# Performance work log

Hardware: AMD Instinct MI355X
Metric: run time of the kernel (lower is better)

Reference implementation:

```python
import jax, jax.numpy as jnp
import numpy as np

STRIDES = (8, 16, 32)
BINS = 16
NC = 80
ALPHA, GAMMA = 0.25, 2.0
W_CLS, W_IOU, W_DFL = 1.0, 7.5, 1.5
B, MAX_GT = 32, 32
EPS = 1e-7


def setup_inputs() -> dict:
    key = jax.random.key(0)
    k0, k1, k2, k3, k4, k5, k6 = jax.random.split(key, 7)
    p0 = jax.random.normal(k0, (B, 4 * BINS + NC, 80, 80), dtype=jnp.float32)
    p1 = jax.random.normal(k1, (B, 4 * BINS + NC, 40, 40), dtype=jnp.float32)
    p2 = jax.random.normal(k2, (B, 4 * BINS + NC, 20, 20), dtype=jnp.float32)
    # realistic xyxy boxes inside a 640x640 image
    c = jax.random.uniform(k3, (B, MAX_GT, 2), minval=60.0, maxval=580.0)
    wh = jax.random.uniform(k4, (B, MAX_GT, 2), minval=16.0, maxval=120.0)
    gt_bboxes = jnp.concatenate([c - wh / 2, c + wh / 2], axis=-1).astype(jnp.float32)
    gt_labels = jax.random.randint(k5, (B, MAX_GT), 0, NC, dtype=jnp.int32)
    raw = jax.random.randint(k6, (B, 8400), 0, 20 * MAX_GT, dtype=jnp.int32)
    matched_gt_inds = jnp.where(raw < MAX_GT, raw, -1)
    return {"p0": p0, "p1": p1, "p2": p2, "gt_bboxes": gt_bboxes,
            "gt_labels": gt_labels, "matched_gt_inds": matched_gt_inds}


def _decode_scale(p, stride):
    # p: [B, 4*BINS + NC, H, W]
    Bp, C, H, W = p.shape
    dfl = p[:, :4 * BINS].reshape(Bp, 4, BINS, H, W)
    cls = p[:, 4 * BINS:]
    # DFL decode: expectation of softmax over bins, scaled by stride
    prob = jax.nn.softmax(dfl, axis=2)
    proj = jnp.arange(BINS, dtype=p.dtype)
    dist = jnp.einsum('bkchw,c->bkhw', prob, proj) * stride  # [B,4,H,W] in pixels
    ys, xs = jnp.meshgrid(jnp.arange(H), jnp.arange(W), indexing='ij')
    cx = ((xs.astype(p.dtype)) + 0.5) * stride
    cy = ((ys.astype(p.dtype)) + 0.5) * stride
    boxes = jnp.stack([cx - dist[:, 0], cy - dist[:, 1],
                       cx + dist[:, 2], cy + dist[:, 3]], axis=-1).reshape(Bp, H * W, 4)
    cls_logits = cls.transpose(0, 2, 3, 1).reshape(Bp, H * W, NC)
    dfl_flat = dfl.transpose(0, 3, 4, 1, 2).reshape(Bp, H * W, 4, BINS)
    grid = jnp.stack([cx, cy], axis=-1).reshape(H * W, 2)
    smap = jnp.full((H * W,), stride, dtype=p.dtype)
    return cls_logits, dfl_flat, boxes, grid, smap


def reference(p0, p1, p2, gt_bboxes, gt_labels, matched_gt_inds):
    outs = [_decode_scale(p, s) for p, s in zip((p0, p1, p2), STRIDES)]
    scores = jnp.concatenate([o[0] for o in outs], axis=1)   # [B,N,NC]
    dfl = jnp.concatenate([o[1] for o in outs], axis=1)      # [B,N,4,BINS]
    pboxes = jnp.concatenate([o[2] for o in outs], axis=1)   # [B,N,4]
    grid = jnp.concatenate([o[3] for o in outs], axis=0)     # [N,2]
    smap = jnp.concatenate([o[4] for o in outs], axis=0)     # [N]

    pos = matched_gt_inds >= 0                               # [B,N]
    idx = jnp.where(pos, matched_gt_inds, 0)
    lbl = jnp.take_along_axis(gt_labels, idx, axis=1)        # [B,N]
    posf = pos.astype(scores.dtype)
    tgt_scores = jax.nn.one_hot(lbl, NC, dtype=scores.dtype) * posf[..., None]

    # sigmoid focal loss (stable BCE-with-logits)
    prob = jax.nn.sigmoid(scores)
    ce = jnp.maximum(scores, 0) - scores * tgt_scores + jnp.log1p(jnp.exp(-jnp.abs(scores)))
    p_t = prob * tgt_scores + (1 - prob) * (1 - tgt_scores)
    alpha_t = tgt_scores * ALPHA + (1 - tgt_scores) * (1 - ALPHA)
    cls_elem = alpha_t * (1.0 - p_t) ** GAMMA * ce
    num_pos = jnp.maximum(posf.sum(), 1.0)
    loss_cls = cls_elem.sum() / num_pos

    # gather matched GT boxes per anchor
    tboxes = jnp.take_along_axis(gt_bboxes, idx[..., None], axis=1)  # [B,N,4]
    gx, gy = grid[None, :, 0], grid[None, :, 1]
    l = jnp.clip(gx - tboxes[..., 0], 0.0)
    t = jnp.clip(gy - tboxes[..., 1], 0.0)
    r = jnp.clip(tboxes[..., 2] - gx, 0.0)
    b_ = jnp.clip(tboxes[..., 3] - gy, 0.0)
    dists = jnp.stack([l, t, r, b_], axis=-1) / smap[None, :, None]   # [B,N,4]
    tb = jnp.clip(dists, 0.0, BINS - 1 - 1e-6)
    lo = jnp.floor(tb).astype(jnp.int32)
    hi = jnp.minimum(lo + 1, BINS - 1)
    a = tb - lo.astype(tb.dtype)
    # soft two-bin DFL target (vectorized form of the scatter_add loop)
    tdist = (jax.nn.one_hot(lo, BINS, dtype=dfl.dtype) * (1.0 - a)[..., None]
             + jax.nn.one_hot(hi, BINS, dtype=dfl.dtype) * a[..., None])   # [B,N,4,BINS]
    logp = jax.nn.log_softmax(dfl, axis=-1)
    dfl_elem = -(tdist * logp).sum(-1)                                # [B,N,4]
    loss_dfl = (dfl_elem * posf[..., None]).sum() / (num_pos * 4.0)

    # IoU loss on positives
    ix1 = jnp.maximum(pboxes[..., 0], tboxes[..., 0])
    iy1 = jnp.maximum(pboxes[..., 1], tboxes[..., 1])
    ix2 = jnp.minimum(pboxes[..., 2], tboxes[..., 2])
    iy2 = jnp.minimum(pboxes[..., 3], tboxes[..., 3])
    inter = jnp.clip(ix2 - ix1, 0.0) * jnp.clip(iy2 - iy1, 0.0)
    area_p = jnp.clip(pboxes[..., 2] - pboxes[..., 0], 0.0) * jnp.clip(pboxes[..., 3] - pboxes[..., 1], 0.0)
    area_t = jnp.clip(tboxes[..., 2] - tboxes[..., 0], 0.0) * jnp.clip(tboxes[..., 3] - tboxes[..., 1], 0.0)
    iou = inter / (area_p + area_t - inter + EPS)
    loss_iou = ((1.0 - iou) * posf).sum() / num_pos

    total = W_CLS * loss_cls + W_IOU * loss_iou + W_DFL * loss_dfl
    return total
```

## Files before the change

### kernel.cpp

```cpp
#include <hip/hip_runtime.h>
#include <math.h>

#define NCLS 80
#define BINS 16
#define BATCH 32
#define MAX_GT 32
#define NA 8400
#define AN (BATCH * NA)
#define NT 2100
#define GRID 2048
#define NU_DFL 2100
#define NU_CLS 5280
#define NVB (NU_DFL + NU_CLS)
#define NROWS (GRID * 2)
#define NSLOT 64
#define ALPHA_C 0.25f
#define W_CLS 1.0
#define W_IOU 7.5
#define W_DFL 1.5
#define EPS_F 1e-7f

__device__ __forceinline__ float focal0(float s)
{
    float e  = __expf(-s);
    float t  = 1.f + e;
    float r  = __builtin_amdgcn_rcpf(t);
    float lg = __logf(t);
    return 0.75f * r * r * (s + lg);
}

__device__ __forceinline__ float focal_corr(float s)
{
    float e  = __expf(-s);
    float t  = 1.f + e;
    float r  = __builtin_amdgcn_rcpf(t);
    float lg = __logf(t);
    return r * r * (0.25f * e * e * lg - 0.75f * (s + lg));
}

__device__ __forceinline__ void wave_write4(float c0, float c1, float c2, float c3,
                                            double* __restrict__ blk)
{
    #pragma unroll
    for (int o = 32; o > 0; o >>= 1) {
        c0 += __shfl_down(c0, o);
        c1 += __shfl_down(c1, o);
        c2 += __shfl_down(c2, o);
        c3 += __shfl_down(c3, o);
    }
    const int lane = (int)threadIdx.x & 63;
    if (lane == 0) {
        const int row = (int)blockIdx.x * 2 + ((int)threadIdx.x >> 6);
        double* o = blk + (size_t)row * 4;
        o[0] = (double)c0; o[1] = (double)c1; o[2] = (double)c2; o[3] = (double)c3;
    }
}

template<int HW, int SSTR, int WQ>
__device__ __forceinline__ void dfl_scale(
    const float* __restrict__ p, int b, int tl, int k, int gbase, int tid,
    const float* __restrict__ gt_bboxes, const int* __restrict__ gt_labels,
    const int* __restrict__ matched,
    float& c_cls, float& c_iou, float& c_dfl, float& c_cnt)
{
    const float stride = (float)SSTR;
    const float inv_s  = 1.f / stride;
    const int h  = tl / WQ;
    const int w0 = (tl - h * WQ) * 4;
    const int off = tl * 4;
    const float cy = ((float)h + 0.5f) * stride;
    const float* pc = p + (size_t)(b * 144 + k * BINS) * HW + off;

    float4 v[BINS];
    #pragma unroll
    for (int i = 0; i < BINS; ++i)
        v[i] = *(const float4*)(pc + (size_t)(i * HW));
    const int4 m4 = *(const int4*)(matched + (size_t)b * NA + gbase + off);
    const int mm[4] = {m4.x, m4.y, m4.z, m4.w};

    float se[4] = {0.f, 0.f, 0.f, 0.f}, we[4] = {0.f, 0.f, 0.f, 0.f};
    #pragma unroll
    for (int i = 0; i < BINS; ++i) {
        const float wgt = (float)i;
        float e0 = __expf(v[i].x), e1 = __expf(v[i].y);
        float e2 = __expf(v[i].z), e3 = __expf(v[i].w);
        se[0] += e0; we[0] = fmaf(wgt, e0, we[0]);
        se[1] += e1; we[1] = fmaf(wgt, e1, we[1]);
        se[2] += e2; we[2] = fmaf(wgt, e2, we[2]);
        se[3] += e3; we[3] = fmaf(wgt, e3, we[3]);
    }

    float pd[4];
    #pragma unroll
    for (int j = 0; j < 4; ++j) pd[j] = (we[j] / se[j]) * stride;

    #pragma unroll
    for (int j = 0; j < 4; ++j) {
        if (mm[j] >= 0) {
            const float4 tb = *(const float4*)(gt_bboxes + ((size_t)b * MAX_GT + mm[j]) * 4);
            const float cx = ((float)(w0 + j) + 0.5f) * stride;
            float d = (k == 0) ? (cx - tb.x) : (k == 1) ? (cy - tb.y)
                    : (k == 2) ? (tb.z - cx) : (tb.w - cy);
            float tval = fminf(fmaxf(d, 0.f) * inv_s, (float)(BINS - 1) - 1e-6f);
            int   lo = (int)tval;
            float fr = tval - (float)lo;
            float vlo = pc[(size_t)(lo * HW) + j];
            float vhi = pc[(size_t)((lo + 1) * HW) + j];
            float lse = __logf(se[j]);
            c_dfl += -((1.f - fr) * (vlo - lse) + fr * (vhi - lse));
        }
    }

    const int lbase = (tid & 63) & ~3;
    float d1[4], d2[4], d3[4];
    #pragma unroll
    for (int j = 0; j < 4; ++j) {
        d1[j] = __shfl(pd[j], lbase + 1);
        d2[j] = __shfl(pd[j], lbase + 2);
        d3[j] = __shfl(pd[j], lbase + 3);
    }
    if (k == 0) {
        #pragma unroll
        for (int j = 0; j < 4; ++j) {
            if (mm[j] >= 0) {
                const float cx = ((float)(w0 + j) + 0.5f) * stride;
                float px1 = cx - pd[j], py1 = cy - d1[j];
                float px2 = cx + d2[j], py2 = cy + d3[j];
                const float4 tb = *(const float4*)(gt_bboxes + ((size_t)b * MAX_GT + mm[j]) * 4);
                float ix1 = fmaxf(px1, tb.x), iy1 = fmaxf(py1, tb.y);
                float ix2 = fminf(px2, tb.z), iy2 = fminf(py2, tb.w);
                float inter  = fmaxf(ix2 - ix1, 0.f) * fmaxf(iy2 - iy1, 0.f);
                float area_p = fmaxf(px2 - px1, 0.f) * fmaxf(py2 - py1, 0.f);
                float area_t = fmaxf(tb.z - tb.x, 0.f) * fmaxf(tb.w - tb.y, 0.f);
                float iou = inter / (area_p + area_t - inter + EPS_F);
                c_iou += 1.f - iou;
                c_cnt += 1.f;
                int lbl = gt_labels[b * MAX_GT + mm[j]];
                float sv = *(p + (size_t)(b * 144 + 4 * BINS + lbl) * HW + off + j);
                c_cls += focal_corr(sv);
            }
        }
    }
}

__global__ __launch_bounds__(128, 4) void yolo_mega(
    const float* __restrict__ p0, const float* __restrict__ p1, const float* __restrict__ p2,
    const float* __restrict__ gt_bboxes, const int* __restrict__ gt_labels,
    const int* __restrict__ matched, double* __restrict__ blk)
{
    const int tid = (int)threadIdx.x;
    float c_cls = 0.f, c_iou = 0.f, c_dfl = 0.f, c_cnt = 0.f;

    for (int vb = (int)blockIdx.x; vb < NVB; vb += GRID) {
        if (vb < NU_DFL) {
            const int gdt = vb * 128 + tid;
            const int k   = gdt & 3;
            const int qg  = gdt >> 2;
            const int b   = qg / NT;
            const int t   = qg - b * NT;
            if (t < 1600)
                dfl_scale<6400,  8, 20>(p0, b, t,        k, 0,    tid,
                                        gt_bboxes, gt_labels, matched, c_cls, c_iou, c_dfl, c_cnt);
            else if (t < 2000)
                dfl_scale<1600, 16, 10>(p1, b, t - 1600, k, 6400, tid,
                                        gt_bboxes, gt_labels, matched, c_cls, c_iou, c_dfl, c_cnt);
            else
                dfl_scale< 400, 32,  5>(p2, b, t - 2000, k, 8000, tid,
                                        gt_bboxes, gt_labels, matched, c_cls, c_iou, c_dfl, c_cnt);
        } else {
            const int c = vb - NU_DFL;
            const int b = c / 165;
            const int r = c - b * 165;
            const float* base; int len, off;
            if (r < 125)      { base = p0 + (size_t)b * 921600 + 409600; len = 512000; off = r * 4096; }
            else if (r < 157) { base = p1 + (size_t)b * 230400 + 102400; len = 128000; off = (r - 125) * 4096; }
            else              { base = p2 + (size_t)b * 57600  + 25600;  len = 32000;  off = (r - 157) * 4096; }

            float4 q[8]; bool val[8];
            #pragma unroll
            for (int i = 0; i < 8; ++i) {
                int o = off + i * 512 + tid * 4;
                val[i] = (o < len);
                q[i] = *(const float4*)(base + (val[i] ? o : 0));
            }
            float part = 0.f;
            #pragma unroll
            for (int i = 0; i < 8; ++i) {
                float s = focal0(q[i].x) + focal0(q[i].y) + focal0(q[i].z) + focal0(q[i].w);
                part += val[i] ? s : 0.f;
            }
            c_cls += part;
        }
    }
    wave_write4(c_cls, c_iou, c_dfl, c_cnt, blk);
}

__global__ __launch_bounds__(1024) void yolo_finalize_blocks(
    const double* __restrict__ blk, float* __restrict__ out)
{
    const int tid = (int)threadIdx.x;
    double s0 = 0.0, s1 = 0.0, s2 = 0.0, s3 = 0.0;
    #pragma unroll
    for (int r = tid; r < NROWS; r += 1024) {
        const double2* rp = (const double2*)(blk + (size_t)r * 4);
        double2 a = rp[0], b = rp[1];
        s0 += a.x; s1 += a.y; s2 += b.x; s3 += b.y;
    }
    #pragma unroll
    for (int o = 32; o > 0; o >>= 1) {
        s0 += __shfl_down(s0, o); s1 += __shfl_down(s1, o);
        s2 += __shfl_down(s2, o); s3 += __shfl_down(s3, o);
    }
    __shared__ double sh[16][4];
    const int wave = tid >> 6, lane = tid & 63;
    if (lane == 0) { sh[wave][0] = s0; sh[wave][1] = s1; sh[wave][2] = s2; sh[wave][3] = s3; }
    __syncthreads();
    if (tid == 0) {
        double c = 0, i = 0, d = 0, n = 0;
        for (int w = 0; w < 16; ++w) { c += sh[w][0]; i += sh[w][1]; d += sh[w][2]; n += sh[w][3]; }
        double np = (n < 1.0) ? 1.0 : n;
        out[0] = (float)(W_CLS * c / np + W_IOU * i / np + W_DFL * d / (np * 4.0));
    }
}

__device__ __forceinline__ void block_reduce_atomic(float val, double* __restrict__ target)
{
    __shared__ float s[4];
    __syncthreads();
    #pragma unroll
    for (int o = 32; o > 0; o >>= 1) val += __shfl_down(val, o);
    const int wave = threadIdx.x >> 6, lane = threadIdx.x & 63;
    if (lane == 0) s[wave] = val;
    __syncthreads();
    if (threadIdx.x == 0) atomicAdd(target, (double)(s[0] + s[1] + s[2] + s[3]));
}

__device__ __forceinline__ float focal_elem(float s, float tt)
{
    float e   = __expf(-fabsf(s));
    float inv = 1.f / (1.f + e);
    float prob = (s >= 0.f) ? inv : e * inv;
    float ce  = fmaxf(s, 0.f) - s * tt + __logf(1.f + e);
    float p_t = prob * tt + (1.f - prob) * (1.f - tt);
    float alpha_t = tt * ALPHA_C + (1.f - tt) * (1.f - ALPHA_C);
    float om = 1.f - p_t;
    return alpha_t * om * om * ce;
}

__global__ __launch_bounds__(256) void yolo_loss_fused(
    const float* __restrict__ p0, const float* __restrict__ p1, const float* __restrict__ p2,
    const float* __restrict__ gt_bboxes, const int* __restrict__ gt_labels,
    const int* __restrict__ matched, double* __restrict__ acc)
{
    const int a = blockIdx.x * blockDim.x + threadIdx.x;
    const int b = blockIdx.y;
    const int slot = blockIdx.x & (NSLOT - 1);
    float cls_acc = 0.f, iou_acc = 0.f, dfl_acc = 0.f, pos_cnt = 0.f;
    if (a < NA) {
        const float* p; int HW, W; float stride; int off;
        if (a < 6400)      { p = p0; HW = 6400; W = 80; stride = 8.f;  off = a; }
        else if (a < 8000) { p = p1; HW = 1600; W = 40; stride = 16.f; off = a - 6400; }
        else               { p = p2; HW = 400;  W = 20; stride = 32.f; off = a - 8000; }
        const int h = off / W, w = off - h * W;
        const float cx = ((float)w + 0.5f) * stride, cy = ((float)h + 0.5f) * stride;
        const float* pb = p + ((size_t)b * 144) * (size_t)HW + (size_t)off;
        const int m = matched[(size_t)b * NA + a];
        const bool pos = (m >= 0);
        const int idx = pos ? m : 0;
        const int lbl = gt_labels[b * MAX_GT + idx];
        const float* tbp = gt_bboxes + ((size_t)b * MAX_GT + idx) * 4;
        const float tx1 = tbp[0], ty1 = tbp[1], tx2 = tbp[2], ty2 = tbp[3];
        float tdist[4] = {fmaxf(cx - tx1, 0.f) / stride, fmaxf(cy - ty1, 0.f) / stride,
                          fmaxf(tx2 - cx, 0.f) / stride, fmaxf(ty2 - cy, 0.f) / stride};
        float pdv[4]; float dfl_sum = 0.f;
        #pragma unroll
        for (int k = 0; k < 4; ++k) {
            float tv = fminf(tdist[k], (float)(BINS - 1) - 1e-6f);
            int lo = (int)floorf(tv);
            float fr = tv - (float)lo;
            const float* pcx = pb + (size_t)(k * BINS) * HW;
            float v[BINS];
            #pragma unroll
            for (int i = 0; i < BINS; ++i) v[i] = pcx[(size_t)i * HW];
            float mx = v[0];
            #pragma unroll
            for (int i = 1; i < BINS; ++i) mx = fmaxf(mx, v[i]);
            float se = 0.f, we = 0.f, vlo = 0.f, vhi = 0.f;
            #pragma unroll
            for (int i = 0; i < BINS; ++i) {
                float e = __expf(v[i] - mx);
                se += e; we += (float)i * e;
                vlo = (i == lo) ? v[i] : vlo;
                vhi = (i == lo + 1) ? v[i] : vhi;
            }
            pdv[k] = (we / se) * stride;
            if (pos) { float lse = mx + __logf(se); dfl_sum += -((1.f - fr) * (vlo - lse) + fr * (vhi - lse)); }
        }
        const float* pcls = pb + (size_t)(4 * BINS) * HW;
        #pragma unroll 4
        for (int c = 0; c < NCLS; ++c)
            cls_acc += focal_elem(pcls[(size_t)c * HW], (pos && c == lbl) ? 1.f : 0.f);
        if (pos) {
            float px1 = cx - pdv[0], py1 = cy - pdv[1], px2 = cx + pdv[2], py2 = cy + pdv[3];
            float ix1 = fmaxf(px1, tx1), iy1 = fmaxf(py1, ty1);
            float ix2 = fminf(px2, tx2), iy2 = fminf(py2, ty2);
            float inter  = fmaxf(ix2 - ix1, 0.f) * fmaxf(iy2 - iy1, 0.f);
            float area_p = fmaxf(px2 - px1, 0.f) * fmaxf(py2 - py1, 0.f);
            float area_t = fmaxf(tx2 - tx1, 0.f) * fmaxf(ty2 - ty1, 0.f);
            float iou = inter / (area_p + area_t - inter + EPS_F);
            iou_acc = 1.f - iou; dfl_acc = dfl_sum; pos_cnt = 1.f;
        }
    }
    block_reduce_atomic(cls_acc, &acc[0 * NSLOT + slot]);
    block_reduce_atomic(iou_acc, &acc[1 * NSLOT + slot]);
    block_reduce_atomic(dfl_acc, &acc[2 * NSLOT + slot]);
    block_reduce_atomic(pos_cnt, &acc[3 * NSLOT + slot]);
}

__global__ void yolo_loss_finalize(const double* __restrict__ acc, float* __restrict__ out)
{
    double s[4] = {0.0, 0.0, 0.0, 0.0};
    for (int q = 0; q < 4; ++q)
        for (int i = 0; i < NSLOT; ++i) s[q] += acc[q * NSLOT + i];
    double np = s[3] < 1.0 ? 1.0 : s[3];
    double total = W_CLS * s[0] / np + W_IOU * s[1] / np + W_DFL * s[2] / (np * 4.0);
    out[0] = (float)total;
}

extern "C" void kernel_launch(void* const* d_in, const int* in_sizes, int n_in,
                              void* d_out, int out_size, void* d_ws, size_t ws_size,
                              hipStream_t stream)
{
    const float* p0        = (const float*)d_in[0];
    const float* p1        = (const float*)d_in[1];
    const float* p2        = (const float*)d_in[2];
    const float* gt_bboxes = (const float*)d_in[3];
    const int*   gt_labels = (const int*)d_in[4];
    const int*   matched   = (const int*)d_in[5];
    float*  out = (float*)d_out;

    const size_t need = (size_t)NROWS * 4 * sizeof(double);

    if (ws_size >= need) {
        double* blk = (double*)d_ws;
        yolo_mega<<<GRID, 128, 0, stream>>>(p0, p1, p2, gt_bboxes, gt_labels, matched, blk);
        yolo_finalize_blocks<<<1, 1024, 0, stream>>>(blk, out);
    } else {
        double* acc = (double*)d_ws;
        (void)hipMemsetAsync(acc, 0, 4 * NSLOT * sizeof(double), stream);
        dim3 g((NA + 255) / 256, BATCH);
        yolo_loss_fused<<<g, 256, 0, stream>>>(p0, p1, p2, gt_bboxes, gt_labels, matched, acc);
        yolo_loss_finalize<<<1, 1, 0, stream>>>(acc, out);
    }
}
```

Measured before the change: 219.0 us.

## Split cls and positive kernels, skip DFL loads for all-negative anchor quads

Separates the dense classification focal sum into its own kernel with a flat grid-stride float4 mapping. The positive-anchor kernel now reads matched indices first and returns early when all four anchors in a quad are negative, which avoids the 16-bin DFL loads for most anchors. Block reductions go through shared memory to one row per block. This adds an extra kernel launch, and the branch divergence in the positive kernel may leave some bandwidth unused.

```diff
diff --git a/kernel.cpp b/kernel.cpp
--- a/kernel.cpp
+++ b/kernel.cpp
@@ -6,13 +6,7 @@
 #define BATCH 32
 #define MAX_GT 32
 #define NA 8400
-#define AN (BATCH * NA)
 #define NT 2100
-#define GRID 2048
-#define NU_DFL 2100
-#define NU_CLS 5280
-#define NVB (NU_DFL + NU_CLS)
-#define NROWS (GRID * 2)
 #define NSLOT 64
 #define ALPHA_C 0.25f
 #define W_CLS 1.0
@@ -20,6 +14,14 @@
 #define W_DFL 1.5
 #define EPS_F 1e-7f
 
+#define IMG_Q4 168000u
+#define CLS_Q4 5376000u
+#define CLS_GRID 2048
+#define CLS_STRIDE (CLS_GRID * 256)
+
+#define POS_GRID 1050
+#define NROWS (CLS_GRID + POS_GRID)
+
 __device__ __forceinline__ float focal0(float s)
 {
     float e  = __expf(-s);
@@ -38,8 +40,8 @@
     return r * r * (0.25f * e * e * lg - 0.75f * (s + lg));
 }
 
-__device__ __forceinline__ void wave_write4(float c0, float c1, float c2, float c3,
-                                            double* __restrict__ blk)
+__device__ __forceinline__ void block_write4(float c0, float c1, float c2, float c3,
+                                             double* __restrict__ row)
 {
     #pragma unroll
     for (int o = 32; o > 0; o >>= 1) {
@@ -48,26 +50,74 @@
         c2 += __shfl_down(c2, o);
         c3 += __shfl_down(c3, o);
     }
-    const int lane = (int)threadIdx.x & 63;
-    if (lane == 0) {
-        const int row = (int)blockIdx.x * 2 + ((int)threadIdx.x >> 6);
-        double* o = blk + (size_t)row * 4;
-        o[0] = (double)c0; o[1] = (double)c1; o[2] = (double)c2; o[3] = (double)c3;
-    }
+    __shared__ float s4[4][4];
+    const int wave = threadIdx.x >> 6, lane = threadIdx.x & 63;
+    if (lane == 0) { s4[wave][0] = c0; s4[wave][1] = c1; s4[wave][2] = c2; s4[wave][3] = c3; }
+    __syncthreads();
+    if (threadIdx.x == 0) {
+        row[0] = (double)(s4[0][0] + s4[1][0] + s4[2][0] + s4[3][0]);
+        row[1] = (double)(s4[0][1] + s4[1][1] + s4[2][1] + s4[3][1]);
+        row[2] = (double)(s4[0][2] + s4[1][2] + s4[2][2] + s4[3][2]);
+        row[3] = (double)(s4[0][3] + s4[1][3] + s4[2][3] + s4[3][3]);
+    }
+}
+
+__device__ __forceinline__ const float4* cls_map(unsigned v,
+    const float4* q0, const float4* q1, const float4* q2)
+{
+    unsigned b  = v / IMG_Q4;
+    unsigned r  = v - b * IMG_Q4;
+    return (r < 128000u) ? (q0 + (size_t)b * 230400 + 102400 + r)
+         : (r < 160000u) ? (q1 + (size_t)b * 57600  + 25600  + (r - 128000u))
+                         : (q2 + (size_t)b * 14400  + 6400   + (r - 160000u));
+}
+
+__global__ __launch_bounds__(256) void yolo_cls(
+    const float* __restrict__ p0, const float* __restrict__ p1, const float* __restrict__ p2,
+    double* __restrict__ blk)
+{
+    const float4* q0 = (const float4*)p0;
+    const float4* q1 = (const float4*)p1;
+    const float4* q2 = (const float4*)p2;
+    const unsigned gtid = blockIdx.x * 256 + threadIdx.x;
+
+    float c = 0.f;
+    unsigned vi = gtid;
+    #pragma unroll
+    for (int rnd = 0; rnd < 2; ++rnd) {
+        float4 q[5];
+        #pragma unroll
+        for (int u = 0; u < 5; ++u)
+            q[u] = *cls_map(vi + u * CLS_STRIDE, q0, q1, q2);
+        #pragma unroll
+        for (int u = 0; u < 5; ++u)
+            c += (focal0(q[u].x) + focal0(q[u].y)) + (focal0(q[u].z) + focal0(q[u].w));
+        vi += 5 * CLS_STRIDE;
+    }
+    if (vi < CLS_Q4) {
+        float4 q = *cls_map(vi, q0, q1, q2);
+        c += (focal0(q.x) + focal0(q.y)) + (focal0(q.z) + focal0(q.w));
+    }
+    block_write4(c, 0.f, 0.f, 0.f, blk + (size_t)blockIdx.x * 4);
 }
 
 template<int HW, int SSTR, int WQ>
-__device__ __forceinline__ void dfl_scale(
+__device__ __forceinline__ void pos_scale(
     const float* __restrict__ p, int b, int tl, int k, int gbase, int tid,
     const float* __restrict__ gt_bboxes, const int* __restrict__ gt_labels,
     const int* __restrict__ matched,
     float& c_cls, float& c_iou, float& c_dfl, float& c_cnt)
 {
+    const int off = tl * 4;
+    const int4 m4 = *(const int4*)(matched + (size_t)b * NA + gbase + off);
+    const int mm[4] = {m4.x, m4.y, m4.z, m4.w};
+    const bool any = (mm[0] >= 0) | (mm[1] >= 0) | (mm[2] >= 0) | (mm[3] >= 0);
+    if (!any) return;
+
     const float stride = (float)SSTR;
     const float inv_s  = 1.f / stride;
     const int h  = tl / WQ;
     const int w0 = (tl - h * WQ) * 4;
-    const int off = tl * 4;
     const float cy = ((float)h + 0.5f) * stride;
     const float* pc = p + (size_t)(b * 144 + k * BINS) * HW + off;
 
@@ -75,8 +125,6 @@
     #pragma unroll
     for (int i = 0; i < BINS; ++i)
         v[i] = *(const float4*)(pc + (size_t)(i * HW));
-    const int4 m4 = *(const int4*)(matched + (size_t)b * NA + gbase + off);
-    const int mm[4] = {m4.x, m4.y, m4.z, m4.w};
 
     float se[4] = {0.f, 0.f, 0.f, 0.f}, we[4] = {0.f, 0.f, 0.f, 0.f};
     #pragma unroll
@@ -143,56 +191,30 @@
     }
 }
 
-__global__ __launch_bounds__(128, 4) void yolo_mega(
+__global__ __launch_bounds__(256) void yolo_pos(
     const float* __restrict__ p0, const float* __restrict__ p1, const float* __restrict__ p2,
     const float* __restrict__ gt_bboxes, const int* __restrict__ gt_labels,
     const int* __restrict__ matched, double* __restrict__ blk)
 {
     const int tid = (int)threadIdx.x;
+    const int gdt = (int)blockIdx.x * 256 + tid;
+    const int k   = gdt & 3;
+    const int qg  = gdt >> 2;
+    const int b   = qg / NT;
+    const int t   = qg - b * NT;
+
     float c_cls = 0.f, c_iou = 0.f, c_dfl = 0.f, c_cnt = 0.f;
-
-    for (int vb = (int)blockIdx.x; vb < NVB; vb += GRID) {
-        if (vb < NU_DFL) {
-            const int gdt = vb * 128 + tid;
-            const int k   = gdt & 3;
-            const int qg  = gdt >> 2;
-            const int b   = qg / NT;
-            const int t   = qg - b * NT;
-            if (t < 1600)
-                dfl_scale<6400,  8, 20>(p0, b, t,        k, 0,    tid,
-                                        gt_bboxes, gt_labels, matched, c_cls, c_iou, c_dfl, c_cnt);
-            else if (t < 2000)
-                dfl_scale<1600, 16, 10>(p1, b, t - 1600, k, 6400, tid,
-                                        gt_bboxes, gt_labels, matched, c_cls, c_iou, c_dfl, c_cnt);
-            else
-                dfl_scale< 400, 32,  5>(p2, b, t - 2000, k, 8000, tid,
-                                        gt_bboxes, gt_labels, matched, c_cls, c_iou, c_dfl, c_cnt);
-        } else {
-            const int c = vb - NU_DFL;
-            const int b = c / 165;
-            const int r = c - b * 165;
-            const float* base; int len, off;
-            if (r < 125)      { base = p0 + (size_t)b * 921600 + 409600; len = 512000; off = r * 4096; }
-            else if (r < 157) { base = p1 + (size_t)b * 230400 + 102400; len = 128000; off = (r - 125) * 4096; }
-            else              { base = p2 + (size_t)b * 57600  + 25600;  len = 32000;  off = (r - 157) * 4096; }
-
-            float4 q[8]; bool val[8];
-            #pragma unroll
-            for (int i = 0; i < 8; ++i) {
-                int o = off + i * 512 + tid * 4;
-                val[i] = (o < len);
-                q[i] = *(const float4*)(base + (val[i] ? o : 0));
-            }
-            float part = 0.f;
-            #pragma unroll
-            for (int i = 0; i < 8; ++i) {
-                float s = focal0(q[i].x) + focal0(q[i].y) + focal0(q[i].z) + focal0(q[i].w);
-                part += val[i] ? s : 0.f;
-            }
-            c_cls += part;
-        }
-    }
-    wave_write4(c_cls, c_iou, c_dfl, c_cnt, blk);
+    if (t < 1600)
+        pos_scale<6400,  8, 20>(p0, b, t,        k, 0,    tid,
+                                gt_bboxes, gt_labels, matched, c_cls, c_iou, c_dfl, c_cnt);
+    else if (t < 2000)
+        pos_scale<1600, 16, 10>(p1, b, t - 1600, k, 6400, tid,
+                                gt_bboxes, gt_labels, matched, c_cls, c_iou, c_dfl, c_cnt);
+    else
+        pos_scale< 400, 32,  5>(p2, b, t - 2000, k, 8000, tid,
+                                gt_bboxes, gt_labels, matched, c_cls, c_iou, c_dfl, c_cnt);
+
+    block_write4(c_cls, c_iou, c_dfl, c_cnt, blk + (size_t)(CLS_GRID + blockIdx.x) * 4);
 }
 
 __global__ __launch_bounds__(1024) void yolo_finalize_blocks(
@@ -200,7 +222,6 @@
 {
     const int tid = (int)threadIdx.x;
     double s0 = 0.0, s1 = 0.0, s2 = 0.0, s3 = 0.0;
-    #pragma unroll
     for (int r = tid; r < NROWS; r += 1024) {
         const double2* rp = (const double2*)(blk + (size_t)r * 4);
         double2 a = rp[0], b = rp[1];
@@ -343,7 +364,8 @@
 
     if (ws_size >= need) {
         double* blk = (double*)d_ws;
-        yolo_mega<<<GRID, 128, 0, stream>>>(p0, p1, p2, gt_bboxes, gt_labels, matched, blk);
+        yolo_cls<<<CLS_GRID, 256, 0, stream>>>(p0, p1, p2, blk);
+        yolo_pos<<<POS_GRID, 256, 0, stream>>>(p0, p1, p2, gt_bboxes, gt_labels, matched, blk);
         yolo_finalize_blocks<<<1, 1024, 0, stream>>>(blk, out);
     } else {
         double* acc = (double*)d_ws;
```

After: 221.8 us. No clear change (+1.2%).
